# Kernel optimization log

Measured on AMD Instinct MI355X. Metric: run time of the kernel, lower is better.

## Reference

```python
import jax, jax.numpy as jnp
import numpy as np

HEADS = 16
THETA = 10000.0


def _rope(x):
    # lucidrains rotary_embedding_torch, interleaved-pair convention, dim = full hidden size
    b, n, d = x.shape
    half = d // 2
    inv_freq = 1.0 / (THETA ** (jnp.arange(0, d, 2, dtype=jnp.float32) / d))  # (half,)
    ang = jnp.arange(n, dtype=jnp.float32)[:, None] * inv_freq               # (n, half)
    cos, sin = jnp.cos(ang), jnp.sin(ang)
    xp = x.reshape(b, n, half, 2)
    x1, x2 = xp[..., 0], xp[..., 1]
    out = jnp.stack([x1 * cos - x2 * sin, x2 * cos + x1 * sin], axis=-1)
    return out.reshape(b, n, d)


def setup_inputs() -> dict:
    key = jax.random.key(0)
    ks = jax.random.split(key, 8)
    B, N, C = 8, 2048, 1024
    s = C ** -0.5
    return {
        "x": jax.random.normal(ks[0], (B, N, C), jnp.float32),
        "Wq": jax.random.normal(ks[1], (C, C), jnp.float32) * s,
        "bq": jax.random.normal(ks[2], (C,), jnp.float32) * 0.01,
        "Wk": jax.random.normal(ks[3], (C, C), jnp.float32) * s,
        "bk": jax.random.normal(ks[4], (C,), jnp.float32) * 0.01,
        "Wv": jax.random.normal(ks[5], (C, C), jnp.float32) * s,
        "bv": jax.random.normal(ks[6], (C,), jnp.float32) * 0.01,
        "gamma": jnp.ones((C,), jnp.float32),
        "beta": jnp.zeros((C,), jnp.float32),
    }


def reference(x, Wq, bq, Wk, bk, Wv, bv, gamma, beta):
    b, n, c = x.shape
    h = HEADS
    d = c // h
    gelu = lambda t: jax.nn.gelu(t, approximate=False)  # torch nn.GELU default = exact erf

    q = gelu(x @ Wq.T + bq) + 0.21
    k = gelu(x @ Wk.T + bk) + 0.21
    v = x @ Wv.T + bv

    q_r = _rope(q)
    k_r = _rope(k)

    split = lambda t: t.reshape(b, n, h, d).transpose(0, 2, 1, 3)  # (b,h,n,d)
    qh, kh, vh, qrh, krh = split(q), split(k), split(v), split(q_r), split(k_r)

    # z = 1 / (q @ mean_n(k)^T + 1e-6), shape (b,h,n,1)
    z = 1.0 / (jnp.einsum('bhnd,bhd->bhn', qh, kh.mean(axis=2)) + 1e-6)

    # kv = (k_rope^T * n^-0.5) @ (v * n^-0.5) -> (b,h,d,d)
    scale = n ** (-0.5)
    kv = jnp.einsum('bhnd,bhne->bhde', krh * scale, vh * scale)

    out = jnp.einsum('bhnd,bhde->bhne', qrh, kv) * z[..., None]  # (b,h,n,d)
    out = out.transpose(0, 2, 1, 3).reshape(b, n, c)

    # dropout is identity at eval; residual + LayerNorm(eps=1e-12)
    res = out + x
    mu = res.mean(-1, keepdims=True)
    var = res.var(-1, keepdims=True)  # biased variance, matches torch LayerNorm
    return (res - mu) / jnp.sqrt(var + 1e-12) * gamma + beta
```

## Files before the change

### kernel.cpp

```cpp
#include <hip/hip_runtime.h>
#include <cstdint>
#include <cstddef>

#define NB 8
#define SEQ 2048
#define CH 1024
#define NH 16
#define HD 64
#define MROWS (NB*SEQ)
#define HALFC 512

typedef __attribute__((ext_vector_type(4))) float f32x4;
typedef __attribute__((ext_vector_type(8))) short s16x8;

__device__ __forceinline__ ushort f2bf(float f) {
    union { float f; unsigned u; } v; v.f = f;
    unsigned r = (v.u + 0x7FFFu + ((v.u >> 16) & 1u)) >> 16;
    return (ushort)r;
}
__device__ __forceinline__ float bf2f(ushort u) {
    union { unsigned u; float f; } v; v.u = ((unsigned)u) << 16;
    return v.f;
}
__device__ __forceinline__ void gload16(const void* g, void* l) {
    __builtin_amdgcn_global_load_lds((const __attribute__((address_space(1))) unsigned*)g,
                                     (__attribute__((address_space(3))) unsigned*)l, 16, 0, 0);
}

__global__ void cvt_bf16_kernel(const float* __restrict__ src, ushort* __restrict__ dst, int n4) {
    int i = blockIdx.x * 256 + threadIdx.x;
    if (i >= n4) return;
    f32x4 v = ((const f32x4*)src)[i];
    ushort4 o;
    o.x = f2bf(v[0]); o.y = f2bf(v[1]); o.z = f2bf(v[2]); o.w = f2bf(v[3]);
    ((ushort4*)dst)[i] = o;
}

__global__ void rope_table_kernel(float* __restrict__ cosT, float* __restrict__ sinT) {
    int idx = blockIdx.x * 256 + threadIdx.x;
    int n = idx >> 9;
    int i = idx & 511;
    float freq = powf(10000.f, -(float)i * (1.f / 512.f));
    float a = (float)n * freq;
    float s, c;
    sincosf(a, &s, &c);
    cosT[idx] = c; sinT[idx] = s;
}

__global__ __launch_bounds__(256, 2) void qkv_gemm_kernel(
    const ushort* __restrict__ xb, const ushort* __restrict__ wb,
    const float* __restrict__ bq, const float* __restrict__ bk, const float* __restrict__ bv,
    const float* __restrict__ cosT, const float* __restrict__ sinT,
    ushort* __restrict__ qr, ushort* __restrict__ kr, ushort* __restrict__ vo,
    float* __restrict__ ksum)
{
    __shared__ ushort As[128 * 64];
    __shared__ ushort Bs[128 * 64];
    const int z = blockIdx.z;
    const ushort* w = wb + (size_t)z * CH * CH;
    const float* bias = (z == 0) ? bq : (z == 1) ? bk : bv;
    ushort* dst = (z == 0) ? qr : (z == 1) ? kr : vo;
    const int row0 = blockIdx.y * 128;
    const int col0 = blockIdx.x * 128;
    const int tid = threadIdx.x;
    const int lane = tid & 63;
    const int wid = tid >> 6;
    const int wm = (wid >> 1) * 64;
    const int wn = (wid & 1) * 64;

    f32x4 acc[4][4] = {};

    for (int kt = 0; kt < CH; kt += 64) {
        __syncthreads();
        #pragma unroll
        for (int i = 0; i < 4; ++i) {
            int cl = i * 256 + tid;
            int r = cl >> 3, ci = cl & 7;
            int sci = ci ^ (r & 7);
            gload16(xb + (size_t)(row0 + r) * CH + kt + sci * 8, (void*)&As[cl * 8]);
            gload16(w  + (size_t)(col0 + r) * CH + kt + sci * 8, (void*)&Bs[cl * 8]);
        }
        asm volatile("s_waitcnt vmcnt(0)" ::: "memory");
        __syncthreads();
        #pragma unroll
        for (int ks = 0; ks < 2; ++ks) {
            s16x8 af[4], bfr[4];
            #pragma unroll
            for (int mi = 0; mi < 4; ++mi) {
                int r = wm + mi * 16 + (lane & 15);
                int ch = ((lane >> 4) + ks * 4) ^ (r & 7);
                af[mi] = *(const s16x8*)&As[r * 64 + ch * 8];
            }
            #pragma unroll
            for (int ni = 0; ni < 4; ++ni) {
                int r = wn + ni * 16 + (lane & 15);
                int ch = ((lane >> 4) + ks * 4) ^ (r & 7);
                bfr[ni] = *(const s16x8*)&Bs[r * 64 + ch * 8];
            }
            #pragma unroll
            for (int mi = 0; mi < 4; ++mi)
                #pragma unroll
                for (int ni = 0; ni < 4; ++ni)
                    acc[mi][ni] = __builtin_amdgcn_mfma_f32_16x16x32_bf16(af[mi], bfr[ni], acc[mi][ni], 0, 0, 0);
        }
    }

    const int bidx = row0 >> 11;
    #pragma unroll
    for (int ni = 0; ni < 4; ++ni) {
        const int cg = col0 + wn + ni * 16 + (lane & 15);
        const float bsv = bias[cg];
        float cs = 0.f;
        #pragma unroll
        for (int mi = 0; mi < 4; ++mi) {
            const int mbase = row0 + wm + mi * 16 + ((lane >> 4) << 2);
            #pragma unroll
            for (int r = 0; r < 4; ++r) {
                float t = acc[mi][ni][r] + bsv;
                float val;
                if (z == 2) {
                    val = t;
                } else {
                    val = 0.5f * t * (1.f + erff(t * 0.7071067811865475f)) + 0.21f;
                }
                if (z == 1) cs += val;
                if (z != 2) {
                    float p = __shfl_xor(val, 1);
                    int n = (mbase + r) & (SEQ - 1);
                    float cv = cosT[n * HALFC + (cg >> 1)];
                    float sv = sinT[n * HALFC + (cg >> 1)];
                    val = (cg & 1) ? (p * sv + val * cv) : (val * cv - p * sv);
                }
                dst[(size_t)(mbase + r) * CH + cg] = f2bf(val);
            }
        }
        if (z == 1) {
            cs += __shfl_xor(cs, 16);
            cs += __shfl_xor(cs, 32);
            if (lane < 16) atomicAdd(&ksum[bidx * CH + cg], cs);
        }
    }
}

__global__ void z_kernel(const ushort* __restrict__ qr, const float* __restrict__ ksum,
                         const float* __restrict__ cosT, const float* __restrict__ sinT,
                         float* __restrict__ zout)
{
    int idx = blockIdx.x * 256 + threadIdx.x;
    int h = idx & 15;
    int m = idx >> 4;
    int b = m >> 11;
    int n = m & (SEQ - 1);
    const ushort* qp = qr + (size_t)m * CH + h * HD;
    const float* kmp = ksum + b * CH + h * HD;
    const float* cp = cosT + (size_t)n * HALFC + h * 32;
    const float* sp = sinT + (size_t)n * HALFC + h * 32;
    float dot = 0.f;
    #pragma unroll
    for (int i = 0; i < 32; ++i) {
        float c = cp[i], s = sp[i];
        float km0 = kmp[2 * i], km1 = kmp[2 * i + 1];
        float q0 = bf2f(qp[2 * i]), q1 = bf2f(qp[2 * i + 1]);
        dot += q0 * (km0 * c - km1 * s) + q1 * (km0 * s + km1 * c);
    }
    dot *= (1.f / 2048.f);
    zout[((size_t)(b * NH + h)) * SEQ + n] = 1.f / (dot + 1e-6f);
}

__global__ __launch_bounds__(256, 2) void kv_partial_kernel(
    const ushort* __restrict__ kr, const ushort* __restrict__ vo, float* __restrict__ kvp)
{
    const int blk = blockIdx.x;
    const int chunk = blk & 7;
    const int bh = blk >> 3;
    const int b = bh >> 4, h = bh & 15;
    __shared__ float ks[64 * 68];
    __shared__ float vs[64 * 68];
    const int tid = threadIdx.x;
    const int d0 = (tid >> 4) * 4;
    const int e0 = (tid & 15) * 4;
    float acc[4][4] = {};
    const size_t base = ((size_t)b * SEQ + chunk * 256) * CH + h * HD;
    const int lrow = tid >> 2;
    const int lcol = (tid & 3) * 16;

    for (int it = 0; it < 4; ++it) {
        __syncthreads();
        const ushort* gk = kr + base + (size_t)(it * 64 + lrow) * CH + lcol;
        const ushort* gv = vo + base + (size_t)(it * 64 + lrow) * CH + lcol;
        s16x8 ka = *(const s16x8*)gk, kb2 = *(const s16x8*)(gk + 8);
        s16x8 va = *(const s16x8*)gv, vb2 = *(const s16x8*)(gv + 8);
        #pragma unroll
        for (int seg = 0; seg < 2; ++seg) {
            s16x8 kk = seg ? kb2 : ka;
            s16x8 vv = seg ? vb2 : va;
            #pragma unroll
            for (int q = 0; q < 2; ++q) {
                f32x4 tk, tv;
                #pragma unroll
                for (int e = 0; e < 4; ++e) {
                    tk[e] = bf2f((ushort)kk[q * 4 + e]);
                    tv[e] = bf2f((ushort)vv[q * 4 + e]);
                }
                *(f32x4*)&ks[lrow * 68 + lcol + seg * 8 + q * 4] = tk;
                *(f32x4*)&vs[lrow * 68 + lcol + seg * 8 + q * 4] = tv;
            }
        }
        __syncthreads();
        for (int n = 0; n < 64; ++n) {
            f32x4 kq = *(const f32x4*)&ks[n * 68 + d0];
            f32x4 vq = *(const f32x4*)&vs[n * 68 + e0];
            #pragma unroll
            for (int di = 0; di < 4; ++di)
                #pragma unroll
                for (int ej = 0; ej < 4; ++ej)
                    acc[di][ej] += kq[di] * vq[ej];
        }
    }
    float* op = kvp + (size_t)blk * 4096;
    #pragma unroll
    for (int di = 0; di < 4; ++di) {
        f32x4 t;
        t[0] = acc[di][0]; t[1] = acc[di][1]; t[2] = acc[di][2]; t[3] = acc[di][3];
        *(f32x4*)&op[(d0 + di) * 64 + e0] = t;
    }
}

__global__ void kv_reduce_kernel(const float* __restrict__ kvp, ushort* __restrict__ kvT) {
    int idx = blockIdx.x * 256 + threadIdx.x;
    int bh = idx >> 12;
    int de = idx & 4095;
    int e = de >> 6, d = de & 63;
    float s = 0.f;
    #pragma unroll
    for (int c = 0; c < 8; ++c)
        s += kvp[((size_t)bh * 8 + c) * 4096 + d * 64 + e];
    kvT[idx] = f2bf(s * (1.f / 2048.f));
}

__global__ __launch_bounds__(256, 2) void pv_kernel(
    const ushort* __restrict__ qr, const ushort* __restrict__ kvT,
    const float* __restrict__ zin, ushort* __restrict__ o)
{
    __shared__ ushort As[128 * 64];
    __shared__ ushort Bs[64 * 64];
    const int bh = blockIdx.y;
    const int b = bh >> 4, h = bh & 15;
    const int row0 = blockIdx.x * 128;
    const int tid = threadIdx.x;
    const int lane = tid & 63, wid = tid >> 6;
    const size_t grow = (size_t)b * SEQ + row0;

    #pragma unroll
    for (int i = 0; i < 4; ++i) {
        int cl = i * 256 + tid;
        int r = cl >> 3, ci = cl & 7;
        int sci = ci ^ (r & 7);
        gload16(qr + (grow + r) * CH + h * HD + sci * 8, (void*)&As[cl * 8]);
    }
    #pragma unroll
    for (int i = 0; i < 2; ++i) {
        int cl = i * 256 + tid;
        int r = cl >> 3, ci = cl & 7;
        int sci = ci ^ (r & 7);
        gload16(kvT + (size_t)bh * 4096 + r * 64 + sci * 8, (void*)&Bs[cl * 8]);
    }
    asm volatile("s_waitcnt vmcnt(0)" ::: "memory");
    __syncthreads();

    f32x4 acc[2][4] = {};
    #pragma unroll
    for (int ks = 0; ks < 2; ++ks) {
        s16x8 af[2], bfr[4];
        #pragma unroll
        for (int mi = 0; mi < 2; ++mi) {
            int r = wid * 32 + mi * 16 + (lane & 15);
            int ch = ((lane >> 4) + ks * 4) ^ (r & 7);
            af[mi] = *(const s16x8*)&As[r * 64 + ch * 8];
        }
        #pragma unroll
        for (int ni = 0; ni < 4; ++ni) {
            int e = ni * 16 + (lane & 15);
            int ch = ((lane >> 4) + ks * 4) ^ (e & 7);
            bfr[ni] = *(const s16x8*)&Bs[e * 64 + ch * 8];
        }
        #pragma unroll
        for (int mi = 0; mi < 2; ++mi)
            #pragma unroll
            for (int ni = 0; ni < 4; ++ni)
                acc[mi][ni] = __builtin_amdgcn_mfma_f32_16x16x32_bf16(af[mi], bfr[ni], acc[mi][ni], 0, 0, 0);
    }

    const float* zp = zin + (size_t)bh * SEQ + row0;
    #pragma unroll
    for (int mi = 0; mi < 2; ++mi) {
        int mb = wid * 32 + mi * 16 + ((lane >> 4) << 2);
        #pragma unroll
        for (int r = 0; r < 4; ++r) {
            float zv = zp[mb + r];
            #pragma unroll
            for (int ni = 0; ni < 4; ++ni) {
                int e = ni * 16 + (lane & 15);
                o[(grow + mb + r) * CH + h * HD + e] = f2bf(acc[mi][ni][r] * zv);
            }
        }
    }
}

__global__ __launch_bounds__(256) void ln_kernel(
    const ushort* __restrict__ o, const float* __restrict__ x,
    const float* __restrict__ gamma, const float* __restrict__ beta,
    float* __restrict__ out)
{
    const int row = blockIdx.x;
    const int tid = threadIdx.x;
    const size_t base = (size_t)row * CH + tid * 4;
    f32x4 xv = *(const f32x4*)(x + base);
    ushort4 ov = *(const ushort4*)(o + base);
    float v0 = bf2f(ov.x) + xv[0];
    float v1 = bf2f(ov.y) + xv[1];
    float v2 = bf2f(ov.z) + xv[2];
    float v3 = bf2f(ov.w) + xv[3];
    float s = v0 + v1 + v2 + v3;
    float q = v0 * v0 + v1 * v1 + v2 * v2 + v3 * v3;
    #pragma unroll
    for (int off = 1; off < 64; off <<= 1) {
        s += __shfl_xor(s, off);
        q += __shfl_xor(q, off);
    }
    __shared__ float red[8];
    int wv = tid >> 6;
    if ((tid & 63) == 0) { red[wv] = s; red[4 + wv] = q; }
    __syncthreads();
    s = red[0] + red[1] + red[2] + red[3];
    q = red[4] + red[5] + red[6] + red[7];
    float mean = s * (1.f / 1024.f);
    float var = q * (1.f / 1024.f) - mean * mean;
    float rstd = rsqrtf(var + 1e-12f);
    f32x4 gv = *(const f32x4*)(gamma + tid * 4);
    f32x4 bv = *(const f32x4*)(beta + tid * 4);
    f32x4 res;
    res[0] = (v0 - mean) * rstd * gv[0] + bv[0];
    res[1] = (v1 - mean) * rstd * gv[1] + bv[1];
    res[2] = (v2 - mean) * rstd * gv[2] + bv[2];
    res[3] = (v3 - mean) * rstd * gv[3] + bv[3];
    *(f32x4*)(out + base) = res;
}

extern "C" void kernel_launch(void* const* d_in, const int* in_sizes, int n_in,
                              void* d_out, int out_size, void* d_ws, size_t ws_size,
                              hipStream_t stream) {
    const float* x     = (const float*)d_in[0];
    const float* Wq    = (const float*)d_in[1];
    const float* bq    = (const float*)d_in[2];
    const float* Wk    = (const float*)d_in[3];
    const float* bk    = (const float*)d_in[4];
    const float* Wv    = (const float*)d_in[5];
    const float* bv    = (const float*)d_in[6];
    const float* gamma = (const float*)d_in[7];
    const float* beta  = (const float*)d_in[8];
    float* out = (float*)d_out;
    char* ws = (char*)d_ws;

    ushort* xb   = (ushort*)(ws);
    ushort* wb   = (ushort*)(ws + (size_t)38  * 0 + (size_t)32 * 1048576);
    float*  cosT = (float*) (ws + (size_t)38  * 1048576);
    float*  sinT = (float*) (ws + (size_t)42  * 1048576);
    ushort* qr   = (ushort*)(ws + (size_t)46  * 1048576);
    ushort* kr   = (ushort*)(ws + (size_t)78  * 1048576);
    ushort* vo   = (ushort*)(ws + (size_t)110 * 1048576);
    float*  ksum = (float*) (ws + (size_t)142 * 1048576);
    ushort* kvT  = (ushort*)(ws + (size_t)143 * 1048576);
    float*  zbuf = (float*) (ws + (size_t)144 * 1048576);
    float*  kvp  = (float*) (ws + (size_t)145 * 1048576);
    ushort* o    = xb;

    hipMemsetAsync(ksum, 0, NB * CH * sizeof(float), stream);
    cvt_bf16_kernel<<<16384, 256, 0, stream>>>(x, xb, MROWS * CH / 4);
    cvt_bf16_kernel<<<1024, 256, 0, stream>>>(Wq, wb,                 CH * CH / 4);
    cvt_bf16_kernel<<<1024, 256, 0, stream>>>(Wk, wb + CH * CH,       CH * CH / 4);
    cvt_bf16_kernel<<<1024, 256, 0, stream>>>(Wv, wb + 2 * CH * CH,   CH * CH / 4);
    rope_table_kernel<<<SEQ * HALFC / 256, 256, 0, stream>>>(cosT, sinT);
    qkv_gemm_kernel<<<dim3(8, 128, 3), 256, 0, stream>>>(xb, wb, bq, bk, bv, cosT, sinT, qr, kr, vo, ksum);
    z_kernel<<<MROWS * NH / 256, 256, 0, stream>>>(qr, ksum, cosT, sinT, zbuf);
    kv_partial_kernel<<<NB * NH * 8, 256, 0, stream>>>(kr, vo, kvp);
    kv_reduce_kernel<<<NB * NH * 4096 / 256, 256, 0, stream>>>(kvp, kvT);
    pv_kernel<<<dim3(16, 128), 256, 0, stream>>>(qr, kvT, zbuf, o);
    ln_kernel<<<MROWS, 256, 0, stream>>>(o, x, gamma, beta, out);
}
```

Before: 438.2 us.

## Interleave RoPE cos/sin table, use fast erf, and remap GEMM block order

Stores cos and sin as one interleaved float2 table, so the QKV epilogue and z kernel each issue a single load per rotation pair instead of two. Replaces erff in the GELU epilogue with an Abramowitz-Stegun polynomial built on a hardware reciprocal and a fast exp, which cuts ALU cost but adds roughly 1e-7 absolute error. Remaps the linear block id in the QKV GEMM so consecutive blocks cover different row tiles of the same column tile, aiming to improve L2 reuse of weight tiles. The remaining edits are type and variable renames.

```diff
diff --git a/kernel.cpp b/kernel.cpp
--- a/kernel.cpp
+++ b/kernel.cpp
@@ -22,9 +22,23 @@
     union { unsigned u; float f; } v; v.u = ((unsigned)u) << 16;
     return v.f;
 }
-__device__ __forceinline__ void gload16(const void* g, void* l) {
+__device__ __forceinline__ void gload16(const ushort* g, ushort* l) {
     __builtin_amdgcn_global_load_lds((const __attribute__((address_space(1))) unsigned*)g,
                                      (__attribute__((address_space(3))) unsigned*)l, 16, 0, 0);
+}
+
+__device__ __forceinline__ float fast_erf(float x) {
+    float ax = fabsf(x);
+    float d = __fmaf_rn(0.3275911f, ax, 1.f);
+    float t; asm("v_rcp_f32 %0, %1" : "=v"(t) : "v"(d));
+    float p = __fmaf_rn(1.061405429f, t, -1.453152027f);
+    p = __fmaf_rn(p, t, 1.421413741f);
+    p = __fmaf_rn(p, t, -0.284496736f);
+    p = __fmaf_rn(p, t, 0.254829592f);
+    p = p * t;
+    float e = __expf(-ax * ax);
+    float r = 1.f - p * e;
+    return copysignf(r, x);
 }
 
 __global__ void cvt_bf16_kernel(const float* __restrict__ src, ushort* __restrict__ dst, int n4) {
@@ -36,7 +50,7 @@
     ((ushort4*)dst)[i] = o;
 }
 
-__global__ void rope_table_kernel(float* __restrict__ cosT, float* __restrict__ sinT) {
+__global__ void rope_table_kernel(float2* __restrict__ csT) {
     int idx = blockIdx.x * 256 + threadIdx.x;
     int n = idx >> 9;
     int i = idx & 511;
@@ -44,13 +58,13 @@
     float a = (float)n * freq;
     float s, c;
     sincosf(a, &s, &c);
-    cosT[idx] = c; sinT[idx] = s;
+    csT[idx] = make_float2(c, s);
 }
 
 __global__ __launch_bounds__(256, 2) void qkv_gemm_kernel(
     const ushort* __restrict__ xb, const ushort* __restrict__ wb,
     const float* __restrict__ bq, const float* __restrict__ bk, const float* __restrict__ bv,
-    const float* __restrict__ cosT, const float* __restrict__ sinT,
+    const float2* __restrict__ csT,
     ushort* __restrict__ qr, ushort* __restrict__ kr, ushort* __restrict__ vo,
     float* __restrict__ ksum)
 {
@@ -60,8 +74,10 @@
     const ushort* w = wb + (size_t)z * CH * CH;
     const float* bias = (z == 0) ? bq : (z == 1) ? bk : bv;
     ushort* dst = (z == 0) ? qr : (z == 1) ? kr : vo;
-    const int row0 = blockIdx.y * 128;
-    const int col0 = blockIdx.x * 128;
+    const int bid = blockIdx.x + 8 * blockIdx.y;
+    const int l = (bid & 7) * 128 + (bid >> 3);
+    const int row0 = (l >> 3) * 128;
+    const int col0 = (l & 7) * 128;
     const int tid = threadIdx.x;
     const int lane = tid & 63;
     const int wid = tid >> 6;
@@ -77,8 +93,8 @@
             int cl = i * 256 + tid;
             int r = cl >> 3, ci = cl & 7;
             int sci = ci ^ (r & 7);
-            gload16(xb + (size_t)(row0 + r) * CH + kt + sci * 8, (void*)&As[cl * 8]);
-            gload16(w  + (size_t)(col0 + r) * CH + kt + sci * 8, (void*)&Bs[cl * 8]);
+            gload16(xb + (size_t)(row0 + r) * CH + kt + sci * 8, (ushort*)&As[cl * 8]);
+            gload16(w  + (size_t)(col0 + r) * CH + kt + sci * 8, (ushort*)&Bs[cl * 8]);
         }
         asm volatile("s_waitcnt vmcnt(0)" ::: "memory");
         __syncthreads();
@@ -121,15 +137,14 @@
                 if (z == 2) {
                     val = t;
                 } else {
-                    val = 0.5f * t * (1.f + erff(t * 0.7071067811865475f)) + 0.21f;
+                    val = 0.5f * t * (1.f + fast_erf(t * 0.70710678f)) + 0.21f;
                 }
                 if (z == 1) cs += val;
                 if (z != 2) {
                     float p = __shfl_xor(val, 1);
                     int n = (mbase + r) & (SEQ - 1);
-                    float cv = cosT[n * HALFC + (cg >> 1)];
-                    float sv = sinT[n * HALFC + (cg >> 1)];
-                    val = (cg & 1) ? (p * sv + val * cv) : (val * cv - p * sv);
+                    float2 cv = csT[n * HALFC + (cg >> 1)];
+                    val = (cg & 1) ? (p * cv.y + val * cv.x) : (val * cv.x - p * cv.y);
                 }
                 dst[(size_t)(mbase + r) * CH + cg] = f2bf(val);
             }
@@ -143,8 +158,7 @@
 }
 
 __global__ void z_kernel(const ushort* __restrict__ qr, const float* __restrict__ ksum,
-                         const float* __restrict__ cosT, const float* __restrict__ sinT,
-                         float* __restrict__ zout)
+                         const float2* __restrict__ csT, float* __restrict__ zout)
 {
     int idx = blockIdx.x * 256 + threadIdx.x;
     int h = idx & 15;
@@ -153,15 +167,14 @@
     int n = m & (SEQ - 1);
     const ushort* qp = qr + (size_t)m * CH + h * HD;
     const float* kmp = ksum + b * CH + h * HD;
-    const float* cp = cosT + (size_t)n * HALFC + h * 32;
-    const float* sp = sinT + (size_t)n * HALFC + h * 32;
+    const float2* cp = csT + (size_t)n * HALFC + h * 32;
     float dot = 0.f;
     #pragma unroll
     for (int i = 0; i < 32; ++i) {
-        float c = cp[i], s = sp[i];
+        float2 cv = cp[i];
         float km0 = kmp[2 * i], km1 = kmp[2 * i + 1];
         float q0 = bf2f(qp[2 * i]), q1 = bf2f(qp[2 * i + 1]);
-        dot += q0 * (km0 * c - km1 * s) + q1 * (km0 * s + km1 * c);
+        dot += q0 * (km0 * cv.x - km1 * cv.y) + q1 * (km0 * cv.y + km1 * cv.x);
     }
     dot *= (1.f / 2048.f);
     zout[((size_t)(b * NH + h)) * SEQ + n] = 1.f / (dot + 1e-6f);
@@ -256,32 +269,32 @@
         int cl = i * 256 + tid;
         int r = cl >> 3, ci = cl & 7;
         int sci = ci ^ (r & 7);
-        gload16(qr + (grow + r) * CH + h * HD + sci * 8, (void*)&As[cl * 8]);
+        gload16(qr + (grow + r) * CH + h * HD + sci * 8, (ushort*)&As[cl * 8]);
     }
     #pragma unroll
     for (int i = 0; i < 2; ++i) {
         int cl = i * 256 + tid;
         int r = cl >> 3, ci = cl & 7;
         int sci = ci ^ (r & 7);
-        gload16(kvT + (size_t)bh * 4096 + r * 64 + sci * 8, (void*)&Bs[cl * 8]);
+        gload16(kvT + (size_t)bh * 4096 + r * 64 + sci * 8, (ushort*)&Bs[cl * 8]);
     }
     asm volatile("s_waitcnt vmcnt(0)" ::: "memory");
     __syncthreads();
 
     f32x4 acc[2][4] = {};
     #pragma unroll
-    for (int ks = 0; ks < 2; ++ks) {
+    for (int ks2 = 0; ks2 < 2; ++ks2) {
         s16x8 af[2], bfr[4];
         #pragma unroll
         for (int mi = 0; mi < 2; ++mi) {
             int r = wid * 32 + mi * 16 + (lane & 15);
-            int ch = ((lane >> 4) + ks * 4) ^ (r & 7);
+            int ch = ((lane >> 4) + ks2 * 4) ^ (r & 7);
             af[mi] = *(const s16x8*)&As[r * 64 + ch * 8];
         }
         #pragma unroll
         for (int ni = 0; ni < 4; ++ni) {
             int e = ni * 16 + (lane & 15);
-            int ch = ((lane >> 4) + ks * 4) ^ (e & 7);
+            int ch = ((lane >> 4) + ks2 * 4) ^ (e & 7);
             bfr[ni] = *(const s16x8*)&Bs[e * 64 + ch * 8];
         }
         #pragma unroll
@@ -363,9 +376,8 @@
     char* ws = (char*)d_ws;
 
     ushort* xb   = (ushort*)(ws);
-    ushort* wb   = (ushort*)(ws + (size_t)38  * 0 + (size_t)32 * 1048576);
-    float*  cosT = (float*) (ws + (size_t)38  * 1048576);
-    float*  sinT = (float*) (ws + (size_t)42  * 1048576);
+    ushort* wb   = (ushort*)(ws + (size_t)32 * 1048576);
+    float2* csT  = (float2*)(ws + (size_t)38 * 1048576);
     ushort* qr   = (ushort*)(ws + (size_t)46  * 1048576);
     ushort* kr   = (ushort*)(ws + (size_t)78  * 1048576);
     ushort* vo   = (ushort*)(ws + (size_t)110 * 1048576);
@@ -380,9 +392,9 @@
     cvt_bf16_kernel<<<1024, 256, 0, stream>>>(Wq, wb,                 CH * CH / 4);
     cvt_bf16_kernel<<<1024, 256, 0, stream>>>(Wk, wb + CH * CH,       CH * CH / 4);
     cvt_bf16_kernel<<<1024, 256, 0, stream>>>(Wv, wb + 2 * CH * CH,   CH * CH / 4);
-    rope_table_kernel<<<SEQ * HALFC / 256, 256, 0, stream>>>(cosT, sinT);
-    qkv_gemm_kernel<<<dim3(8, 128, 3), 256, 0, stream>>>(xb, wb, bq, bk, bv, cosT, sinT, qr, kr, vo, ksum);
-    z_kernel<<<MROWS * NH / 256, 256, 0, stream>>>(qr, ksum, cosT, sinT, zbuf);
+    rope_table_kernel<<<SEQ * HALFC / 256, 256, 0, stream>>>(csT);
+    qkv_gemm_kernel<<<dim3(8, 128, 3), 256, 0, stream>>>(xb, wb, bq, bk, bv, csT, qr, kr, vo, ksum);
+    z_kernel<<<MROWS * NH / 256, 256, 0, stream>>>(qr, ksum, csT, zbuf);
     kv_partial_kernel<<<NB * NH * 8, 256, 0, stream>>>(kr, vo, kvp);
     kv_reduce_kernel<<<NB * NH * 4096 / 256, 256, 0, stream>>>(kvp, kvT);
     pv_kernel<<<dim3(16, 128), 256, 0, stream>>>(qr, kvT, zbuf, o);
```

Result: faster. 422.8 us (-3.5%).
